# Optimization experiments

Measured on AMD Instinct MI355X. Metric: run time of the kernel, lower is better.

Reference implementation:

```python
import jax, jax.numpy as jnp
import numpy as np

TEMPERATURE = 1.0

def setup_inputs() -> dict:
    key = jax.random.key(0)
    k1, k2, k3 = jax.random.split(key, 3)
    B, N, D = 1024, 256, 512
    return {
        "fg_img_feature": jax.random.normal(k1, (B, D), dtype=jnp.float32),
        "fg_pro_feature": jax.random.normal(k2, (B, D), dtype=jnp.float32),
        "bg_pro_feature": jax.random.normal(k3, (B, N, D), dtype=jnp.float32),
    }

def reference(fg_img_feature, fg_pro_feature, bg_pro_feature):
    # Only the image features are L2-normalized (matches original module).
    img = fg_img_feature / jnp.linalg.norm(fg_img_feature, axis=-1, keepdims=True)  # [B, D]
    # Per-sample scalar logit: img_i . fg_pro_i
    pos_logits = jnp.sum(img * fg_pro_feature, axis=-1) / TEMPERATURE  # [B]
    # Per-sample batched matvec against N background prototypes.
    bg_logits = jnp.einsum('bd,bnd->bn', img, bg_pro_feature) / TEMPERATURE  # [B, N]
    positive_sims = jnp.sum(jnp.exp(pos_logits))
    negative_sims = positive_sims + jnp.sum(jnp.exp(bg_logits))
    return -jnp.log(positive_sims / negative_sims)
```

## Files before the change

kernel.cpp:

```cpp
#include <hip/hip_runtime.h>
#include <hip/hip_bf16.h>
#include <math.h>


#define D_DIM 512

__device__ __forceinline__ float wave_reduce_sum(float x) {
    #pragma unroll
    for (int off = 32; off > 0; off >>= 1)
        x += __shfl_xor(x, off);
    return x;
}

__global__ __launch_bounds__(256) void infonce_main(
    const float* __restrict__ img,
    const float* __restrict__ fg_pro,
    const float* __restrict__ bg_pro,
    float* __restrict__ accum,
    int N)
{
    const int b    = blockIdx.x;
    const int tid  = threadIdx.x;
    const int wid  = tid >> 6;
    const int lane = tid & 63;

    __shared__ float s_img[D_DIM];
    __shared__ float s_red[8];

    const float2 v = reinterpret_cast<const float2*>(img + (size_t)b * D_DIM)[tid];
    float ss = v.x * v.x + v.y * v.y;
    ss = wave_reduce_sum(ss);
    if (lane == 0) s_red[wid] = ss;
    __syncthreads();
    const float sumsq = s_red[0] + s_red[1] + s_red[2] + s_red[3];
    const float inv   = rsqrtf(sumsq);

    const float2 nv = make_float2(v.x * inv, v.y * inv);
    reinterpret_cast<float2*>(s_img)[tid] = nv;

    const float2 p = reinterpret_cast<const float2*>(fg_pro + (size_t)b * D_DIM)[tid];
    float pd = nv.x * p.x + nv.y * p.y;
    pd = wave_reduce_sum(pd);
    if (lane == 0) s_red[4 + wid] = pd;
    __syncthreads();
    if (tid == 0) {
        const float pos = s_red[4] + s_red[5] + s_red[6] + s_red[7];
        atomicAdd(&accum[0], expf(pos));
    }

    const float4* s_img4 = reinterpret_cast<const float4*>(s_img);
    const float4  a0 = s_img4[lane];
    const float4  a1 = s_img4[64 + lane];

    const float4* bg4 = reinterpret_cast<const float4*>(bg_pro + (size_t)b * N * D_DIM);
    float local = 0.0f;
    for (int n = wid; n < N; n += 4) {
        const float4* row = bg4 + (size_t)n * (D_DIM / 4);
        const float4 b0 = row[lane];
        const float4 b1 = row[64 + lane];
        float dot = a0.x * b0.x + a0.y * b0.y + a0.z * b0.z + a0.w * b0.w
                  + a1.x * b1.x + a1.y * b1.y + a1.z * b1.z + a1.w * b1.w;
        dot = wave_reduce_sum(dot);
        if (lane == 0) local += expf(dot);
    }
    if (lane == 0) s_red[wid] = local;
    __syncthreads();
    if (tid == 0)
        atomicAdd(&accum[1], s_red[0] + s_red[1] + s_red[2] + s_red[3]);
}

__global__ void infonce_finalize(const float* __restrict__ accum,
                                 float* __restrict__ out)
{
    const float pos = accum[0];
    const float neg = accum[1];
    out[0] = logf(pos + neg) - logf(pos);
}

extern "C" void kernel_launch(void* const* d_in, const int* in_sizes, int n_in,
                              void* d_out, int out_size, void* d_ws, size_t ws_size,
                              hipStream_t stream)
{
    const float* img = (const float*)d_in[0];
    const float* fg  = (const float*)d_in[1];
    const float* bg  = (const float*)d_in[2];
    float* out   = (float*)d_out;
    float* accum = (float*)d_ws;

    const int B = in_sizes[0] / D_DIM;
    const int N = in_sizes[2] / in_sizes[0];

    hipMemsetAsync(accum, 0, 2 * sizeof(float), stream);
    infonce_main<<<B, 256, 0, stream>>>(img, fg, bg, accum, N);
    infonce_finalize<<<1, 1, 0, stream>>>(accum, out);
}
```

Measured before the change: 685.5 us.

## Split each sample's rows across two blocks and unroll four rows per wave

Launches two blocks per sample, and each block handles half of the background rows. Within a wave the loop now walks contiguous rows four at a time, issuing eight float4 loads before the reductions. This gives more memory parallelism and more blocks in flight for a bandwidth-bound kernel. In exchange, the image normalization is recomputed in both blocks, more atomics hit the shared accumulator, and the code assumes N is divisible by 32.

```diff
diff --git a/kernel.cpp b/kernel.cpp
--- a/kernel.cpp
+++ b/kernel.cpp
@@ -3,14 +3,8 @@
 #include <math.h>
 
 
-#define D_DIM 512
-
-__device__ __forceinline__ float wave_reduce_sum(float x) {
-    #pragma unroll
-    for (int off = 32; off > 0; off >>= 1)
-        x += __shfl_xor(x, off);
-    return x;
-}
+#define D_DIM   512
+#define NSPLIT  2
 
 __global__ __launch_bounds__(256) void infonce_main(
     const float* __restrict__ img,
@@ -19,34 +13,42 @@
     float* __restrict__ accum,
     int N)
 {
-    const int b    = blockIdx.x;
-    const int tid  = threadIdx.x;
-    const int wid  = tid >> 6;
-    const int lane = tid & 63;
+    const int b     = blockIdx.x >> 1;
+    const int split = blockIdx.x & 1;
+    const int tid   = threadIdx.x;
+    const int wid   = tid >> 6;
+    const int lane  = tid & 63;
 
     __shared__ float s_img[D_DIM];
     __shared__ float s_red[8];
 
     const float2 v = reinterpret_cast<const float2*>(img + (size_t)b * D_DIM)[tid];
     float ss = v.x * v.x + v.y * v.y;
-    ss = wave_reduce_sum(ss);
+    #pragma unroll
+    for (int off = 32; off > 0; off >>= 1) ss += __shfl_xor(ss, off);
     if (lane == 0) s_red[wid] = ss;
     __syncthreads();
-    const float sumsq = s_red[0] + s_red[1] + s_red[2] + s_red[3];
-    const float inv   = rsqrtf(sumsq);
+    const float inv = rsqrtf(s_red[0] + s_red[1] + s_red[2] + s_red[3]);
 
     const float2 nv = make_float2(v.x * inv, v.y * inv);
     reinterpret_cast<float2*>(s_img)[tid] = nv;
 
-    const float2 p = reinterpret_cast<const float2*>(fg_pro + (size_t)b * D_DIM)[tid];
-    float pd = nv.x * p.x + nv.y * p.y;
-    pd = wave_reduce_sum(pd);
-    if (lane == 0) s_red[4 + wid] = pd;
+    if (split == 0) {
+        const float2 p = reinterpret_cast<const float2*>(fg_pro + (size_t)b * D_DIM)[tid];
+        float pd = nv.x * p.x + nv.y * p.y;
+        #pragma unroll
+        for (int off = 32; off > 0; off >>= 1) pd += __shfl_xor(pd, off);
+        if (lane == 0) s_red[4 + wid] = pd;
+    }
     __syncthreads();
-    if (tid == 0) {
+    if (split == 0 && tid == 0) {
         const float pos = s_red[4] + s_red[5] + s_red[6] + s_red[7];
         atomicAdd(&accum[0], expf(pos));
     }
+
+    const int rows_per_block = N / NSPLIT;
+    const int rows_per_wave  = rows_per_block / 4;
+    const int n0 = split * rows_per_block + wid * rows_per_wave;
 
     const float4* s_img4 = reinterpret_cast<const float4*>(s_img);
     const float4  a0 = s_img4[lane];
@@ -54,15 +56,37 @@
 
     const float4* bg4 = reinterpret_cast<const float4*>(bg_pro + (size_t)b * N * D_DIM);
     float local = 0.0f;
-    for (int n = wid; n < N; n += 4) {
-        const float4* row = bg4 + (size_t)n * (D_DIM / 4);
-        const float4 b0 = row[lane];
-        const float4 b1 = row[64 + lane];
-        float dot = a0.x * b0.x + a0.y * b0.y + a0.z * b0.z + a0.w * b0.w
-                  + a1.x * b1.x + a1.y * b1.y + a1.z * b1.z + a1.w * b1.w;
-        dot = wave_reduce_sum(dot);
-        if (lane == 0) local += expf(dot);
+
+    for (int i = 0; i < rows_per_wave; i += 4) {
+        const float4* r0 = bg4 + (size_t)(n0 + i + 0) * (D_DIM / 4);
+        const float4* r1 = bg4 + (size_t)(n0 + i + 1) * (D_DIM / 4);
+        const float4* r2 = bg4 + (size_t)(n0 + i + 2) * (D_DIM / 4);
+        const float4* r3 = bg4 + (size_t)(n0 + i + 3) * (D_DIM / 4);
+        const float4 b00 = r0[lane], b01 = r0[64 + lane];
+        const float4 b10 = r1[lane], b11 = r1[64 + lane];
+        const float4 b20 = r2[lane], b21 = r2[64 + lane];
+        const float4 b30 = r3[lane], b31 = r3[64 + lane];
+
+        float d0 = a0.x*b00.x + a0.y*b00.y + a0.z*b00.z + a0.w*b00.w
+                 + a1.x*b01.x + a1.y*b01.y + a1.z*b01.z + a1.w*b01.w;
+        float d1 = a0.x*b10.x + a0.y*b10.y + a0.z*b10.z + a0.w*b10.w
+                 + a1.x*b11.x + a1.y*b11.y + a1.z*b11.z + a1.w*b11.w;
+        float d2 = a0.x*b20.x + a0.y*b20.y + a0.z*b20.z + a0.w*b20.w
+                 + a1.x*b21.x + a1.y*b21.y + a1.z*b21.z + a1.w*b21.w;
+        float d3 = a0.x*b30.x + a0.y*b30.y + a0.z*b30.z + a0.w*b30.w
+                 + a1.x*b31.x + a1.y*b31.y + a1.z*b31.z + a1.w*b31.w;
+
+        #pragma unroll
+        for (int off = 32; off > 0; off >>= 1) {
+            d0 += __shfl_xor(d0, off);
+            d1 += __shfl_xor(d1, off);
+            d2 += __shfl_xor(d2, off);
+            d3 += __shfl_xor(d3, off);
+        }
+        if (lane == 0)
+            local += expf(d0) + expf(d1) + expf(d2) + expf(d3);
     }
+
     if (lane == 0) s_red[wid] = local;
     __syncthreads();
     if (tid == 0)
@@ -91,6 +115,6 @@
     const int N = in_sizes[2] / in_sizes[0];
 
     hipMemsetAsync(accum, 0, 2 * sizeof(float), stream);
-    infonce_main<<<B, 256, 0, stream>>>(img, fg, bg, accum, N);
+    infonce_main<<<B * NSPLIT, 256, 0, stream>>>(img, fg, bg, accum, N);
     infonce_finalize<<<1, 1, 0, stream>>>(accum, out);
 }
```

Result: no change. 679.4 us (-0.9%).
